# Performance work log

Measured on AMD Instinct MI355X. Metric: run time of the kernel, lower is better.

## Reference

```python
import jax, jax.numpy as jnp
import numpy as np

T, B, A, N = 64, 32, 8, 16
E, H = 64, 4
LSTM_I, LSTM_H = 128, 128
D_SELF = 16 + 9 * (32 - 2) + 4  # 290


def setup_inputs() -> dict:
    key = jax.random.key(0)
    ks = jax.random.split(key, 24)
    f32 = jnp.float32
    d = {}
    d["x_agent"] = jax.random.normal(ks[0], (T, B, A, 16), f32)
    d["x_lidar"] = jax.random.normal(ks[1], (T, B, A, 32), f32)
    d["x_safe_zone"] = jax.random.normal(ks[2], (T, B, A, 4), f32)
    d["x_ent0"] = jax.random.normal(ks[3], (T, B, A, N, 12), f32)
    d["x_ent1"] = jax.random.normal(ks[4], (T, B, A, N, 8), f32)
    d["mask0"] = jax.random.randint(ks[5], (T, B, A, N), 0, 2).astype(jnp.int32)
    d["mask1"] = jax.random.randint(ks[6], (T, B, A, N), 0, 2).astype(jnp.int32)
    d["done"] = jax.random.randint(ks[7], (T, B), 0, 2).astype(jnp.int32)
    d["actions"] = jax.random.randint(ks[8], (T, B, A, 2), 0, 5).astype(jnp.int32)
    w = lambda k, s: jax.random.normal(k, s, f32) * 0.05
    z = lambda s: jnp.zeros(s, f32)
    d["conv_w"] = w(ks[9], (9, 1, 3)); d["conv_b"] = z((9,))
    d["self_w"] = w(ks[10], (E, 2 * D_SELF)); d["self_b"] = z((E,))
    d["ent0_w"] = w(ks[11], (E, 12 + D_SELF)); d["ent0_b"] = z((E,))
    d["ent1_w"] = w(ks[12], (E, 8 + D_SELF)); d["ent1_b"] = z((E,))
    d["in_proj_w"] = w(ks[13], (3 * E, E)); d["in_proj_b"] = z((3 * E,))
    d["out_proj_w"] = w(ks[14], (E, E)); d["out_proj_b"] = z((E,))
    d["sa_w"] = w(ks[15], (E, E)); d["sa_b"] = z((E,))
    d["pool_w"] = w(ks[16], (LSTM_I, D_SELF + E)); d["pool_b"] = z((LSTM_I,))
    d["w_ih"] = w(ks[17], (4 * LSTM_H, LSTM_I)); d["w_hh"] = w(ks[18], (4 * LSTM_H, LSTM_H))
    d["b_ih"] = z((4 * LSTM_H,)); d["b_hh"] = z((4 * LSTM_H,))
    d["head0_w"] = w(ks[19], (5, LSTM_H)); d["head0_b"] = z((5,))
    d["head1_w"] = w(ks[20], (5, LSTM_H)); d["head1_b"] = z((5,))
    return d


def _forward(x_agent, x_lidar, x_safe_zone, x_ent0, x_ent1,
             conv_w, conv_b, self_w, self_b, ent0_w, ent0_b, ent1_w, ent1_b,
             in_proj_w, in_proj_b, out_proj_w, out_proj_b, sa_w, sa_b,
             pool_w, pool_b, w_ih, w_hh, b_ih, b_hh,
             head0_w, head0_b, head1_w, head1_b,
             mask0, mask1, done, actions):
    f32 = jnp.float32
    lin = lambda x, w, b: x @ w.T + b
    # lidar conv: Conv1d(1,9,k=3), padding=0 (padding_mode='circular' is inert with padding=0)
    xl = x_lidar.reshape(T * B * A, 1, 32)
    zl = jax.lax.conv_general_dilated(xl, conv_w, (1,), 'VALID',
                                      dimension_numbers=('NCH', 'OIH', 'NCH'))
    zl = jax.nn.relu(zl + conv_b[None, :, None]).reshape(T, B, A, -1)  # (T,B,A,270)
    x_self = jnp.concatenate([x_agent, zl, x_safe_zone], axis=-1)  # (T,B,A,290)
    z_self = jax.nn.relu(lin(jnp.concatenate([x_self, x_self], -1), self_w, self_b))[..., None, :]
    xs = jnp.broadcast_to(x_self[..., None, :], (T, B, A, N, D_SELF))
    z0 = jax.nn.relu(lin(jnp.concatenate([x_ent0, xs], -1), ent0_w, ent0_b))
    z1 = jax.nn.relu(lin(jnp.concatenate([x_ent1, xs], -1), ent1_w, ent1_b))
    z_ent = jnp.concatenate([z_self, z0, z1], axis=-2)  # (T,B,A,M,E), M = 1+2N = 33
    M = z_ent.shape[-2]
    mask = jnp.concatenate([jnp.ones((T, B, A, 1), f32),
                            mask0.astype(f32), mask1.astype(f32)], axis=-1)  # (T,B,A,M)
    # self-attention over entities, flattened over (T,B,A)
    S = T * B * A
    zf = z_ent.reshape(S, M, E)
    q, k, v = jnp.split(zf @ in_proj_w.T + in_proj_b, 3, axis=-1)
    Dh = E // H
    q = q.reshape(S, M, H, Dh); k = k.reshape(S, M, H, Dh); v = v.reshape(S, M, H, Dh)
    sc = jnp.einsum('sqhd,skhd->shqk', q, k) / np.float32(np.sqrt(Dh))
    valid = mask.reshape(S, M) > 0
    sc = jnp.where(valid[:, None, None, :], sc, jnp.float32(-1e9))
    attn = jax.nn.softmax(sc, axis=-1)
    o = jnp.einsum('shqk,skhd->sqhd', attn, v).reshape(S, M, E)
    o = (o @ out_proj_w.T + out_proj_b).reshape(T, B, A, M, E)
    res = z_ent + jax.nn.relu(lin(o, sa_w, sa_b))
    z_pool = jnp.mean(res * mask[..., None], axis=-2)  # torch.mean over entity dim (divide by M)
    zin = jax.nn.relu(lin(jnp.concatenate([x_self, z_pool], -1), pool_w, pool_b))  # (T,B,A,128)
    # LSTM scan with done-based state resets (PyTorch gate order i,f,g,o)
    zin_f = zin.reshape(T, B * A, LSTM_I)
    done_f = jnp.repeat(done.astype(f32), A, axis=-1)  # (T, B*A)
    def step(carry, inp):
        h, c = carry
        x_t, d_t = inp
        keep = (1.0 - d_t)[:, None]
        h = h * keep
        c = c * keep
        g = x_t @ w_ih.T + b_ih + h @ w_hh.T + b_hh
        i, f, gg, og = jnp.split(g, 4, axis=-1)
        c = jax.nn.sigmoid(f) * c + jax.nn.sigmoid(i) * jnp.tanh(gg)
        h = jax.nn.sigmoid(og) * jnp.tanh(c)
        return (h, c), h
    h0 = jnp.zeros((B * A, LSTM_H), f32)
    c0 = jnp.zeros((B * A, LSTM_H), f32)
    _, hs = jax.lax.scan(step, (h0, c0), (zin_f, done_f))
    z_lstm = hs.reshape(T, B, A, LSTM_H)
    # categorical heads: per-head logprob of given action and entropy
    lps, ents = [], []
    for i, (hw, hb) in enumerate(((head0_w, head0_b), (head1_w, head1_b))):
        logp = jax.nn.log_softmax(lin(z_lstm, hw, hb), axis=-1)
        p = jnp.exp(logp)
        ents.append(-(p * logp).sum(-1))
        lps.append(jnp.take_along_axis(logp, actions[..., i:i + 1], axis=-1)[..., 0])
    logprobs = lps[0] * lps[1]  # .prod(dim=-1) over heads as in source
    entropies = jnp.stack(ents, axis=-1)
    return logprobs, entropies


def reference(x_agent, x_lidar, x_safe_zone, x_ent0, x_ent1, mask0, mask1, done, actions,
              conv_w, conv_b, self_w, self_b, ent0_w, ent0_b, ent1_w, ent1_b,
              in_proj_w, in_proj_b, out_proj_w, out_proj_b, sa_w, sa_b,
              pool_w, pool_b, w_ih, w_hh, b_ih, b_hh,
              head0_w, head0_b, head1_w, head1_b):
    logprobs, entropies = _forward(x_agent, x_lidar, x_safe_zone, x_ent0, x_ent1,
                                   conv_w, conv_b, self_w, self_b, ent0_w, ent0_b,
                                   ent1_w, ent1_b, in_proj_w, in_proj_b, out_proj_w,
                                   out_proj_b, sa_w, sa_b, pool_w, pool_b,
                                   w_ih, w_hh, b_ih, b_hh,
                                   head0_w, head0_b, head1_w, head1_b,
                                   mask0, mask1, done, actions)
    return (actions, logprobs, entropies)
```

## Files before the change

### kernel.cpp

```cpp
#include <hip/hip_runtime.h>
#include <hip/hip_bf16.h>
#include <math.h>

#define T_DIM 64
#define B_DIM 32
#define S_TOT 16384
#define BA 256
#define FN_SB 16

#define ACT_OFF 0
#define LP_OFF 32768
#define ENT_OFF 49152

typedef __attribute__((ext_vector_type(8))) short short8;
typedef __attribute__((ext_vector_type(4))) float f32x4;
typedef unsigned int uint32;

__device__ __forceinline__ float sigf(float x) { return 1.0f / (1.0f + expf(-x)); }
__device__ __forceinline__ float bf2f(unsigned short u) {
    union { unsigned int i; float f; } a; a.i = ((unsigned int)u) << 16; return a.f;
}
__device__ __forceinline__ uint32 pkbf(float a, float b) {
    __hip_bfloat16 ha = __float2bfloat16(a), hb = __float2bfloat16(b);
    return (uint32)(*(unsigned short*)&ha) | ((uint32)(*(unsigned short*)&hb) << 16);
}
__device__ __forceinline__ short f2bs(float v) {
    __hip_bfloat16 h = __float2bfloat16(v); return *(short*)&h;
}
__device__ __forceinline__ int pswz(int row) { return (((row & 3) ^ ((row >> 2) & 3)) << 4); }

__global__ __launch_bounds__(256) void k_cvt2(
    const float* __restrict__ inp_w, const float* __restrict__ outp_w,
    const float* __restrict__ outp_b, const float* __restrict__ sa_w,
    const float* __restrict__ sa_b, const float* __restrict__ self_w,
    const float* __restrict__ pool_w, const float* __restrict__ ent0_w,
    const float* __restrict__ ent1_w, const float* __restrict__ w_ih,
    const float* __restrict__ w_hh,
    short* __restrict__ wq, short* __restrict__ Wf,
    short* __restrict__ We0, short* __restrict__ We1,
    short* __restrict__ wos, float* __restrict__ bos,
    short* __restrict__ wihb, short* __restrict__ whhb,
    short* __restrict__ wp2)
{
    int i = blockIdx.x * 256 + threadIdx.x;
    if (i < 12288) wq[i] = f2bs(inp_w[i]);
    if (i < 65536) { wihb[i] = f2bs(w_ih[i]); whhb[i] = f2bs(w_hh[i]); }
    if (i < 8192) { int c = i >> 6, k = i & 63; wp2[i] = f2bs(pool_w[(size_t)c * 354 + 290 + k]); }
    if (i < 4096) {
        int c = i >> 6, k = i & 63;
        float s = 0.f;
        for (int j = 0; j < 64; ++j) s = fmaf(sa_w[c * 64 + j], outp_w[j * 64 + k], s);
        wos[i] = f2bs(s);
    }
    if (i < 64) {
        float s = sa_b[i];
        for (int j = 0; j < 64; ++j) s = fmaf(sa_w[i * 64 + j], outp_b[j], s);
        bos[i] = s;
    }
    if (i < 1024) {
        int cp = i >> 4, k = i & 15;
        int ct = cp >> 4, lr2 = cp & 15;
        int e = 32 * (ct >> 1) + 2 * lr2 + (ct & 1);
        We0[i] = f2bs(k < 12 ? ent0_w[e * 302 + k] : 0.f);
        We1[i] = f2bs(k < 8 ? ent1_w[e * 298 + k] : 0.f);
    }
    if (i < 102400) {
        int c = i / 320, k = i - c * 320;
        float v = 0.f;
        if (k < 290) {
            if (c < 64) v = self_w[c * 580 + k] + self_w[c * 580 + 290 + k];
            else if (c < 192) v = pool_w[(size_t)(c - 64) * 354 + k];
            else if (c < 256) v = ent0_w[(c - 192) * 302 + 12 + k];
            else v = ent1_w[(c - 256) * 298 + 8 + k];
        }
        Wf[i] = f2bs(v);
    }
}

#define FN_XSB 0
#define FN_XP0 16384
#define FN_XP1 20736
#define FN_TOTAL 25088

__global__ __launch_bounds__(256, 4) void k_frontN(
    const float* __restrict__ xag, const float* __restrict__ xlid,
    const float* __restrict__ xsz, const float* __restrict__ xe0,
    const float* __restrict__ xe1,
    const float* __restrict__ conv_w, const float* __restrict__ conv_b,
    const float* __restrict__ self_b, const float* __restrict__ ent0_b,
    const float* __restrict__ ent1_b,
    const short* __restrict__ Wf, const short* __restrict__ We0,
    const short* __restrict__ We1,
    __hip_bfloat16* __restrict__ z_ent, float* __restrict__ zin_x)
{
    extern __shared__ char smem[];
    char* xsb = smem + FN_XSB;
    float* xp0f = (float*)(smem + FN_XP0);
    float* xp1f = (float*)(smem + FN_XP1);
    char* ae = smem + FN_XSB;
    float* lidf = (float*)(smem + FN_XP0);

    const int tid = threadIdx.x;
    const int s0 = blockIdx.x * FN_SB;
    const int wv = __builtin_amdgcn_readfirstlane(tid >> 6);
    const int l = tid & 63;
    const int lr = l & 15;
    const int lg = l >> 4;

    for (int i = tid; i < FN_SB * 32; i += 256) {
        int d = i & 31, sl = i >> 5;
        lidf[d * 18 + sl] = xlid[(size_t)s0 * 32 + i];
    }
    for (int i = tid; i < FN_SB * 16; i += 256) {
        int sl = i >> 4, d = i & 15;
        *(short*)(xsb + ((sl * 640 + d * 2) ^ ((sl & 7) << 4))) = f2bs(xag[(size_t)s0 * 16 + i]);
    }
    for (int i = tid; i < FN_SB * 4; i += 256) {
        int sl = i >> 2, d = i & 3;
        *(short*)(xsb + ((sl * 640 + (286 + d) * 2) ^ ((sl & 7) << 4))) = f2bs(xsz[(size_t)s0 * 4 + i]);
    }
    for (int i = tid; i < FN_SB * 30; i += 256) {
        int sl = i / 30, d = 290 + (i - (i / 30) * 30);
        *(short*)(xsb + ((sl * 640 + d * 2) ^ ((sl & 7) << 4))) = 0;
    }
    __syncthreads();
    for (int i = tid; i < 270 * FN_SB; i += 256) {
        int cp = i >> 4, sl = i & 15;
        int c = cp / 30, p = cp - c * 30;
        float v = conv_b[c] + conv_w[c * 3] * lidf[p * 18 + sl]
                + conv_w[c * 3 + 1] * lidf[(p + 1) * 18 + sl]
                + conv_w[c * 3 + 2] * lidf[(p + 2) * 18 + sl];
        *(short*)(xsb + ((sl * 640 + (16 + cp) * 2) ^ ((sl & 7) << 4))) = f2bs(fmaxf(v, 0.f));
    }
    __syncthreads();

    f32x4 acc[5];
    #pragma unroll
    for (int c = 0; c < 5; ++c) acc[c] = (f32x4){0.f, 0.f, 0.f, 0.f};

    for (int kk = 0; kk < 10; ++kk) {
        short8 af = *(const short8*)(xsb + ((lr * 640 + kk * 64 + lg * 16) ^ ((lr & 7) << 4)));
        short8 bf[5];
        #pragma unroll
        for (int c = 0; c < 5; ++c) {
            int col = (wv * 5 + c) * 16 + lr;
            bf[c] = *(const short8*)(Wf + (size_t)col * 320 + kk * 32 + lg * 8);
        }
        #pragma unroll
        for (int c = 0; c < 5; ++c)
            acc[c] = __builtin_amdgcn_mfma_f32_16x16x32_bf16(af, bf[c], acc[c], 0, 0, 0);
    }

    #pragma unroll
    for (int c = 0; c < 5; ++c) {
        int ct = wv * 5 + c;
        int gc = ct * 16 + lr;
        int rowb = lg * 4;
        f32x4 a = acc[c];
        if (ct * 16 < 64) {
            float bias = self_b[gc];
            #pragma unroll
            for (int r = 0; r < 4; ++r)
                z_ent[(size_t)(s0 + rowb + r) * 2112 + gc] = __float2bfloat16(fmaxf(a[r] + bias, 0.f));
        } else if (ct * 16 < 192) {
            int r2 = gc - 64;
            #pragma unroll
            for (int r = 0; r < 4; ++r)
                zin_x[(size_t)(s0 + rowb + r) * 128 + r2] = a[r];
        } else if (ct * 16 < 256) {
            float bias = ent0_b[gc - 192];
            #pragma unroll
            for (int r = 0; r < 4; ++r)
                xp0f[(rowb + r) * 68 + (gc - 192)] = a[r] + bias;
        } else {
            float bias = ent1_b[gc - 256];
            #pragma unroll
            for (int r = 0; r < 4; ++r)
                xp1f[(rowb + r) * 68 + (gc - 256)] = a[r] + bias;
        }
    }
    __syncthreads();

    {
        short8 bz = {0, 0, 0, 0, 0, 0, 0, 0};
        short8 be[4];
        #pragma unroll
        for (int ct = 0; ct < 4; ++ct) {
            int col = ct * 16 + lr;
            short8 bv = *(const short8*)(We0 + col * 16 + (lg & 1) * 8);
            be[ct] = (lg < 2) ? bv : bz;
        }
        for (int i = tid; i < 4096; i += 256) ((uint32*)ae)[i] = 0;
        __syncthreads();
        for (int i = tid; i < FN_SB * 192; i += 256) {
            int sl = i / 192, r = i - sl * 192;
            int n = r / 12, d = r - n * 12;
            int lrow = sl * 16 + n;
            *(short*)(ae + ((lrow * 64 + d * 2) ^ ((lrow & 3) << 4))) =
                f2bs(xe0[(size_t)s0 * 192 + i]);
        }
        __syncthreads();
        #pragma unroll
        for (int j = 0; j < 4; ++j) {
            int gs = wv * 4 + j;
            int row = gs * 16 + lr;
            short8 af = *(const short8*)(ae + ((row * 64 + lg * 16) ^ ((row & 3) << 4)));
            f32x4 a2[4];
            #pragma unroll
            for (int ct = 0; ct < 4; ++ct) {
                f32x4 z = {0.f, 0.f, 0.f, 0.f};
                a2[ct] = __builtin_amdgcn_mfma_f32_16x16x32_bf16(af, be[ct], z, 0, 0, 0);
            }
            #pragma unroll
            for (int t = 0; t < 2; ++t) {
                int e0 = 32 * t + 2 * lr;
                float xv0 = xp0f[gs * 68 + e0];
                float xv1 = xp0f[gs * 68 + e0 + 1];
                #pragma unroll
                for (int r = 0; r < 4; ++r) {
                    int n = lg * 4 + r;
                    float v0 = fmaxf(a2[2 * t][r] + xv0, 0.f);
                    float v1 = fmaxf(a2[2 * t + 1][r] + xv1, 0.f);
                    *(uint32*)((char*)z_ent + ((size_t)(s0 + gs) * 2112 + (1 + n) * 64 + e0) * 2) = pkbf(v0, v1);
                }
            }
        }
        __syncthreads();
    }

    {
        short8 bz = {0, 0, 0, 0, 0, 0, 0, 0};
        short8 be[4];
        #pragma unroll
        for (int ct = 0; ct < 4; ++ct) {
            int col = ct * 16 + lr;
            short8 bv = *(const short8*)(We1 + col * 16 + (lg & 1) * 8);
            be[ct] = (lg < 2) ? bv : bz;
        }
        for (int i = tid; i < 4096; i += 256) ((uint32*)ae)[i] = 0;
        __syncthreads();
        for (int i = tid; i < FN_SB * 128; i += 256) {
            int sl = i >> 7, r = i & 127;
            int n = r >> 3, d = r & 7;
            int lrow = sl * 16 + n;
            *(short*)(ae + ((lrow * 64 + d * 2) ^ ((lrow & 3) << 4))) =
                f2bs(xe1[(size_t)s0 * 128 + i]);
        }
        __syncthreads();
        #pragma unroll
        for (int j = 0; j < 4; ++j) {
            int gs = wv * 4 + j;
            int row = gs * 16 + lr;
            short8 af = *(const short8*)(ae + ((row * 64 + lg * 16) ^ ((row & 3) << 4)));
            f32x4 a2[4];
            #pragma unroll
            for (int ct = 0; ct < 4; ++ct) {
                f32x4 z = {0.f, 0.f, 0.f, 0.f};
                a2[ct] = __builtin_amdgcn_mfma_f32_16x16x32_bf16(af, be[ct], z, 0, 0, 0);
            }
            #pragma unroll
            for (int t = 0; t < 2; ++t) {
                int e0 = 32 * t + 2 * lr;
                float xv0 = xp1f[gs * 68 + e0];
                float xv1 = xp1f[gs * 68 + e0 + 1];
                #pragma unroll
                for (int r = 0; r < 4; ++r) {
                    int n = lg * 4 + r;
                    float v0 = fmaxf(a2[2 * t][r] + xv0, 0.f);
                    float v1 = fmaxf(a2[2 * t + 1][r] + xv1, 0.f);
                    *(uint32*)((char*)z_ent + ((size_t)(s0 + gs) * 2112 + (17 + n) * 64 + e0) * 2) = pkbf(v0, v1);
                }
            }
        }
    }
}

#define AG_QB   0
#define AG_KB   4224
#define AG_VT   8448
#define AG_PW   12544
#define AG_P32  16640
#define AG_V32  17408
#define AG_MSK  17664
#define AG_TOTAL 17824

__global__ __launch_bounds__(256, 8) void k_attnG(
    const __hip_bfloat16* __restrict__ z_ent,
    const int* __restrict__ mask0, const int* __restrict__ mask1,
    const short* __restrict__ wqkvb, const float* __restrict__ inp_b,
    const short* __restrict__ wos_g, const float* __restrict__ bos_g,
    float* __restrict__ pooled_ws)
{
    extern __shared__ char smem[];
    char*  Qb  = smem + AG_QB;
    char*  Kb  = smem + AG_KB;
    char*  Vt  = smem + AG_VT;
    char*  Pw  = smem + AG_PW;
    float* P32 = (float*)(smem + AG_P32);
    float* V32 = (float*)(smem + AG_V32);
    float* msk = (float*)(smem + AG_MSK);
    char*  ob  = Qb;

    const int tid = threadIdx.x;
    const int s = blockIdx.x;
    const short* zg = (const short*)(z_ent + (size_t)s * 2112);

    if (tid < 16) msk[1 + tid] = (float)mask0[(size_t)s * 16 + tid];
    else if (tid < 32) msk[17 + (tid - 16)] = (float)mask1[(size_t)s * 16 + (tid - 16)];
    else if (tid == 32) msk[0] = 1.0f;

    const int wv = __builtin_amdgcn_readfirstlane(tid >> 6);
    const int l  = tid & 63;
    const int lr = l & 15;
    const int lg = l >> 4;

    {
        short8 bw[3][2]; float bias[3];
        #pragma unroll
        for (int c = 0; c < 3; ++c) {
            int col = (wv * 3 + c) * 16 + lr;
            bw[c][0] = *(const short8*)(wqkvb + col * 64 + lg * 8);
            bw[c][1] = *(const short8*)(wqkvb + col * 64 + 32 + lg * 8);
            bias[c] = inp_b[col];
        }
        for (int rt = 0; rt < 3; ++rt) {
            int arow = rt * 16 + lr;
            if (arow > 32) arow = 32;
            short8 a0 = *(const short8*)(zg + arow * 64 + lg * 8);
            short8 a1 = *(const short8*)(zg + arow * 64 + 32 + lg * 8);
            #pragma unroll
            for (int c = 0; c < 3; ++c) {
                f32x4 acc = {0.f, 0.f, 0.f, 0.f};
                acc = __builtin_amdgcn_mfma_f32_16x16x32_bf16(a0, bw[c][0], acc, 0, 0, 0);
                acc = __builtin_amdgcn_mfma_f32_16x16x32_bf16(a1, bw[c][1], acc, 0, 0, 0);
                int col = (wv * 3 + c) * 16 + lr;
                int rb = rt * 16 + lg * 4;
                #pragma unroll
                for (int r = 0; r < 4; ++r) {
                    int q = rb + r;
                    if (q < 33) {
                        float val = acc[r] + bias[c];
                        if (col < 64) {
                            int h = col >> 4, d = col & 15;
                            *(short*)(Qb + ((h * 33 + q) * 32) + d * 2) = f2bs(val);
                        } else if (col < 128) {
                            int kc = col - 64; int h = kc >> 4, d = kc & 15;
                            *(short*)(Kb + ((h * 33 + q) * 32) + d * 2) = f2bs(val);
                        } else {
                            int vc = col - 128; int h = vc >> 4, d = vc & 15;
                            if (q < 32)
                                *(short*)(Vt + (h * 16 + d) * 64 + ((q * 2) ^ pswz(d))) = f2bs(val);
                            else
                                V32[h * 16 + d] = val;
                        }
                    }
                }
            }
        }
    }
    __syncthreads();

    uint32 pk[3][4];
    {
        const short8 zero8 = {0, 0, 0, 0, 0, 0, 0, 0};
        short8 kf[3];
        #pragma unroll
        for (int t = 0; t < 3; ++t)
            kf[t] = (lg < 2) ? *(const short8*)(Kb + ((wv * 33 + t * 16 + lr) * 32) + lg * 16) : zero8;
        float mk0 = msk[lr];
        float mk1 = msk[16 + lr];
        float mk2 = (lr == 0) ? msk[32] : 0.f;
        #pragma unroll
        for (int qt = 0; qt < 3; ++qt) {
            short8 qf = (lg < 2) ? *(const short8*)(Qb + ((wv * 33 + qt * 16 + lr) * 32) + lg * 16) : zero8;
            f32x4 z = {0.f, 0.f, 0.f, 0.f};
            f32x4 S0 = __builtin_amdgcn_mfma_f32_16x16x32_bf16(qf, kf[0], z, 0, 0, 0);
            f32x4 S1 = __builtin_amdgcn_mfma_f32_16x16x32_bf16(qf, kf[1], z, 0, 0, 0);
            f32x4 S2 = __builtin_amdgcn_mfma_f32_16x16x32_bf16(qf, kf[2], z, 0, 0, 0);
            #pragma unroll
            for (int r = 0; r < 4; ++r) {
                float v0 = (mk0 > 0.f) ? S0[r] * 0.25f : -1e9f;
                float v1 = (mk1 > 0.f) ? S1[r] * 0.25f : -1e9f;
                float v2 = (mk2 > 0.f) ? S2[r] * 0.25f : -1e9f;
                float m = fmaxf(fmaxf(v0, v1), v2);
                m = fmaxf(m, __shfl_xor(m, 1));
                m = fmaxf(m, __shfl_xor(m, 2));
                m = fmaxf(m, __shfl_xor(m, 4));
                m = fmaxf(m, __shfl_xor(m, 8));
                float e0 = __expf(v0 - m), e1 = __expf(v1 - m), e2 = __expf(v2 - m);
                float sm = e0 + e1 + e2;
                sm += __shfl_xor(sm, 1);
                sm += __shfl_xor(sm, 2);
                sm += __shfl_xor(sm, 4);
                sm += __shfl_xor(sm, 8);
                float inv = 1.0f / sm;
                pk[qt][r] = pkbf(e0 * inv, e1 * inv);
                if (lr == 0) P32[wv * 48 + qt * 16 + lg * 4 + r] = e2 * inv;
            }
        }
    }
    __syncthreads();

    {
        short8 vf = *(const short8*)(Vt + (wv * 16 + lr) * 64 + ((lg * 16) ^ pswz(lr)));
        float v32reg = V32[wv * 16 + lr];
        f32x4 C[3];
        #pragma unroll
        for (int qt = 0; qt < 3; ++qt) {
            #pragma unroll
            for (int r = 0; r < 4; ++r) {
                int ql = lg * 4 + r;
                uint32 p = pk[qt][r];
                char* prow = Pw + wv * 1024 + ql * 64;
                int sz = pswz(ql);
                *(short*)(prow + ((lr * 2) ^ sz)) = (short)(p & 0xffffu);
                *(short*)(prow + (((16 + lr) * 2) ^ sz)) = (short)(p >> 16);
            }
            short8 pf = *(const short8*)(Pw + wv * 1024 + lr * 64 + ((lg * 16) ^ pswz(lr)));
            f32x4 z = {0.f, 0.f, 0.f, 0.f};
            C[qt] = __builtin_amdgcn_mfma_f32_16x16x32_bf16(pf, vf, z, 0, 0, 0);
        }
        #pragma unroll
        for (int qt = 0; qt < 3; ++qt) {
            #pragma unroll
            for (int r = 0; r < 4; ++r) {
                int q = qt * 16 + lg * 4 + r;
                if (q <= 32) {
                    float cv = C[qt][r] + P32[wv * 48 + q] * v32reg;
                    *(short*)(ob + ((q * 128 + (wv * 16 + lr) * 2) ^ ((q & 7) << 4))) = f2bs(cv);
                }
            }
        }
    }
    __syncthreads();

    {
        int col = wv * 16 + lr;
        short8 b0 = *(const short8*)(wos_g + col * 64 + lg * 8);
        short8 b1 = *(const short8*)(wos_g + col * 64 + 32 + lg * 8);
        float bias = bos_g[col];
        float ps = 0.f;
        for (int rt = 0; rt < 3; ++rt) {
            int arow = rt * 16 + lr;
            int sw = (arow & 7) << 4;
            short8 a0 = *(const short8*)(ob + ((arow * 128 + lg * 16) ^ sw));
            short8 a1 = *(const short8*)(ob + ((arow * 128 + 64 + lg * 16) ^ sw));
            f32x4 acc = {0.f, 0.f, 0.f, 0.f};
            acc = __builtin_amdgcn_mfma_f32_16x16x32_bf16(a0, b0, acc, 0, 0, 0);
            acc = __builtin_amdgcn_mfma_f32_16x16x32_bf16(a1, b1, acc, 0, 0, 0);
            int rb = rt * 16 + lg * 4;
            #pragma unroll
            for (int r = 0; r < 4; ++r) {
                int row = rb + r;
                if (row < 33) {
                    float zev = bf2f(*(const unsigned short*)(zg + row * 64 + col));
                    ps += msk[row] * (zev + fmaxf(acc[r] + bias, 0.f));
                }
            }
        }
        ps += __shfl_xor(ps, 16); ps += __shfl_xor(ps, 32);
        if (lg == 0) pooled_ws[(size_t)s * 64 + col] = ps * (1.0f / 33.0f);
    }
}

__global__ __launch_bounds__(256, 2) void k_zinx(
    const float* __restrict__ pooled_ws, const float* __restrict__ zin_x,
    const short* __restrict__ wp2, const float* __restrict__ pool_b,
    const short* __restrict__ wihb, const float* __restrict__ b_ih,
    const float* __restrict__ b_hh, short* __restrict__ xp)
{
    extern __shared__ char smem[];
    char* A1 = smem;
    char* zt = smem + 8192;
    const int tid = threadIdx.x;
    const size_t r0 = (size_t)blockIdx.x * 64;

    for (int i = tid; i < 2048; i += 256) {
        int sl = i >> 5, dp = i & 31;
        float2 v = ((const float2*)(pooled_ws + (r0 + sl) * 64))[dp];
        *(uint32*)(A1 + ((sl * 128 + dp * 4) ^ ((sl & 7) << 4))) = pkbf(v.x, v.y);
    }
    __syncthreads();

    const int wv = __builtin_amdgcn_readfirstlane(tid >> 6);
    const int l = tid & 63;
    const int lr = l & 15;
    const int lg = l >> 4;

    #pragma unroll
    for (int c = 0; c < 2; ++c) {
        int col = (wv * 2 + c) * 16 + lr;
        short8 bf0 = *(const short8*)(wp2 + col * 64 + lg * 8);
        short8 bf1 = *(const short8*)(wp2 + col * 64 + 32 + lg * 8);
        float bias = pool_b[col];
        #pragma unroll
        for (int rt = 0; rt < 4; ++rt) {
            int row16 = rt * 16 + lr;
            short8 a0 = *(const short8*)(A1 + ((row16 * 128 + lg * 16) ^ ((row16 & 7) << 4)));
            short8 a1 = *(const short8*)(A1 + ((row16 * 128 + 64 + lg * 16) ^ ((row16 & 7) << 4)));
            f32x4 acc = {0.f, 0.f, 0.f, 0.f};
            acc = __builtin_amdgcn_mfma_f32_16x16x32_bf16(a0, bf0, acc, 0, 0, 0);
            acc = __builtin_amdgcn_mfma_f32_16x16x32_bf16(a1, bf1, acc, 0, 0, 0);
            #pragma unroll
            for (int r = 0; r < 4; ++r) {
                int row = rt * 16 + lg * 4 + r;
                float v = fmaxf(acc[r] + bias + zin_x[(r0 + row) * 128 + col], 0.f);
                *(short*)(zt + ((row * 256 + col * 2) ^ ((row & 7) << 4))) = f2bs(v);
            }
        }
    }
    __syncthreads();

    short8 af[4][4];
    #pragma unroll
    for (int rt = 0; rt < 4; ++rt)
        #pragma unroll
        for (int kc = 0; kc < 4; ++kc) {
            int row = rt * 16 + lr;
            af[rt][kc] = *(const short8*)(zt + ((row * 256 + kc * 64 + lg * 16) ^ ((row & 7) << 4)));
        }

    for (int ct8 = 0; ct8 < 8; ++ct8) {
        int ct = wv * 8 + ct8;
        int col = ct * 16 + lr;
        short8 bf[4];
        #pragma unroll
        for (int kc = 0; kc < 4; ++kc)
            bf[kc] = *(const short8*)(wihb + (size_t)col * 128 + kc * 32 + lg * 8);
        float bias = b_ih[col] + b_hh[col];
        int g = col >> 7, j = col & 127;
        #pragma unroll
        for (int rt = 0; rt < 4; ++rt) {
            f32x4 acc = {0.f, 0.f, 0.f, 0.f};
            #pragma unroll
            for (int kc = 0; kc < 4; ++kc)
                acc = __builtin_amdgcn_mfma_f32_16x16x32_bf16(af[rt][kc], bf[kc], acc, 0, 0, 0);
            #pragma unroll
            for (int r = 0; r < 4; ++r)
                xp[(r0 + rt * 16 + lg * 4 + r) * 512 + j * 4 + g] = f2bs(acc[r] + bias);
        }
    }
}

__global__ __launch_bounds__(512, 1) void k_lstm2(
    const short* __restrict__ xp, const short* __restrict__ whhb,
    const int* __restrict__ done, float* __restrict__ h_all)
{
    __shared__ short hl[16 * 128];
    __shared__ float keepl[64 * 16];
    const int tid = threadIdx.x;
    const int s0 = blockIdx.x * 16;
    const int wv = __builtin_amdgcn_readfirstlane(tid >> 6);
    const int l = tid & 63;
    const int lr = l & 15;
    const int lg = l >> 4;

    for (int i = tid; i < 1024; i += 512) {
        int t = i >> 4, ls = i & 15;
        keepl[i] = done[t * 32 + ((s0 + ls) >> 3)] ? 0.f : 1.f;
    }
    for (int i = tid; i < 1024; i += 512) ((uint32*)hl)[i] = 0;

    short8 bf[4][4];
    #pragma unroll
    for (int gi = 0; gi < 4; ++gi) {
        int col = (gi * 8 + wv) * 16 + lr;
        #pragma unroll
        for (int kc = 0; kc < 4; ++kc)
            bf[gi][kc] = *(const short8*)(whhb + (size_t)col * 128 + kc * 32 + lg * 8);
    }
    float c0 = 0.f, c1 = 0.f, c2 = 0.f, c3 = 0.f;
    const int jcol = wv * 16 + lr;

    short4 xn[4];
    #pragma unroll
    for (int r = 0; r < 4; ++r)
        xn[r] = *(const short4*)(xp + ((size_t)(s0 + lg * 4 + r)) * 512 + jcol * 4);
    __syncthreads();

    for (int t = 0; t < T_DIM; ++t) {
        short4 xc[4];
        #pragma unroll
        for (int r = 0; r < 4; ++r) xc[r] = xn[r];
        if (t < 63) {
            #pragma unroll
            for (int r = 0; r < 4; ++r)
                xn[r] = *(const short4*)(xp + ((size_t)(t + 1) * 256 + s0 + lg * 4 + r) * 512 + jcol * 4);
        }
        short8 af[4];
        #pragma unroll
        for (int kc = 0; kc < 4; ++kc)
            af[kc] = *(const short8*)((char*)hl + ((lr * 256 + kc * 64 + lg * 16) ^ ((lr & 7) << 4)));
        f32x4 z = {0.f, 0.f, 0.f, 0.f};
        f32x4 Ci = z, Cf = z, Cg = z, Co = z;
        #pragma unroll
        for (int kc = 0; kc < 4; ++kc) {
            Ci = __builtin_amdgcn_mfma_f32_16x16x32_bf16(af[kc], bf[0][kc], Ci, 0, 0, 0);
            Cf = __builtin_amdgcn_mfma_f32_16x16x32_bf16(af[kc], bf[1][kc], Cf, 0, 0, 0);
            Cg = __builtin_amdgcn_mfma_f32_16x16x32_bf16(af[kc], bf[2][kc], Cg, 0, 0, 0);
            Co = __builtin_amdgcn_mfma_f32_16x16x32_bf16(af[kc], bf[3][kc], Co, 0, 0, 0);
        }
        __syncthreads();

        #pragma unroll
        for (int r = 0; r < 4; ++r) {
            int sl = lg * 4 + r;
            float kt = keepl[t * 16 + sl];
            float gi = bf2f((unsigned short)xc[r].x) + Ci[r];
            float gf = bf2f((unsigned short)xc[r].y) + Cf[r];
            float gg = bf2f((unsigned short)xc[r].z) + Cg[r];
            float go = bf2f((unsigned short)xc[r].w) + Co[r];
            float cc = (r == 0 ? c0 : r == 1 ? c1 : r == 2 ? c2 : c3) * kt;
            cc = sigf(gf) * cc + sigf(gi) * tanhf(gg);
            float hn = sigf(go) * tanhf(cc);
            if (r == 0) c0 = cc; else if (r == 1) c1 = cc; else if (r == 2) c2 = cc; else c3 = cc;
            float kn = (t < 63) ? keepl[(t + 1) * 16 + sl] : 1.f;
            *(short*)((char*)hl + ((sl * 256 + jcol * 2) ^ ((sl & 7) << 4))) = f2bs(hn * kn);
            h_all[((size_t)t * 256 + s0 + sl) * 128 + jcol] = hn;
        }
        __syncthreads();
    }
}

__global__ __launch_bounds__(256) void k_heads(
    const float* __restrict__ h_all, const int* __restrict__ actions,
    const float* __restrict__ h0w, const float* __restrict__ h0b,
    const float* __restrict__ h1w, const float* __restrict__ h1b,
    float* __restrict__ out)
{
    __shared__ float w0[640], w1[640], b0[8], b1[8];
    const int tid = threadIdx.x;
    for (int i = tid; i < 640; i += 256) { w0[i] = h0w[i]; w1[i] = h1w[i]; }
    if (tid < 5) { b0[tid] = h0b[tid]; b1[tid] = h1b[tid]; }
    __syncthreads();
    const int g = blockIdx.x * 256 + tid;
    const float* h = h_all + (size_t)g * 128;
    float l0[5], l1[5];
    #pragma unroll
    for (int cc = 0; cc < 5; ++cc) { l0[cc] = b0[cc]; l1[cc] = b1[cc]; }
    for (int j = 0; j < 128; ++j) {
        float hv = h[j];
        #pragma unroll
        for (int cc = 0; cc < 5; ++cc) {
            l0[cc] = fmaf(w0[cc * 128 + j], hv, l0[cc]);
            l1[cc] = fmaf(w1[cc * 128 + j], hv, l1[cc]);
        }
    }
    int a0 = actions[(size_t)g * 2], a1 = actions[(size_t)g * 2 + 1];
    float m0 = l0[0], m1 = l1[0];
    #pragma unroll
    for (int cc = 1; cc < 5; ++cc) { m0 = fmaxf(m0, l0[cc]); m1 = fmaxf(m1, l1[cc]); }
    float s0 = 0.f, s1 = 0.f;
    #pragma unroll
    for (int cc = 0; cc < 5; ++cc) { s0 += expf(l0[cc] - m0); s1 += expf(l1[cc] - m1); }
    float lse0 = m0 + logf(s0), lse1 = m1 + logf(s1);
    float ent0 = 0.f, ent1 = 0.f, lp0 = 0.f, lp1 = 0.f;
    #pragma unroll
    for (int cc = 0; cc < 5; ++cc) {
        float p0 = l0[cc] - lse0, p1 = l1[cc] - lse1;
        ent0 -= expf(p0) * p0;
        ent1 -= expf(p1) * p1;
        if (cc == a0) lp0 = p0;
        if (cc == a1) lp1 = p1;
    }
    out[ACT_OFF + (size_t)g * 2]     = (float)a0;
    out[ACT_OFF + (size_t)g * 2 + 1] = (float)a1;
    out[LP_OFF + g]                  = lp0 * lp1;
    out[ENT_OFF + (size_t)g * 2]     = ent0;
    out[ENT_OFF + (size_t)g * 2 + 1] = ent1;
}

extern "C" void kernel_launch(void* const* d_in, const int* in_sizes, int n_in,
                              void* d_out, int out_size, void* d_ws, size_t ws_size,
                              hipStream_t stream)
{
    const float* x_agent = (const float*)d_in[0];
    const float* x_lidar = (const float*)d_in[1];
    const float* x_safe  = (const float*)d_in[2];
    const float* x_ent0  = (const float*)d_in[3];
    const float* x_ent1  = (const float*)d_in[4];
    const int*   mask0   = (const int*)d_in[5];
    const int*   mask1   = (const int*)d_in[6];
    const int*   done    = (const int*)d_in[7];
    const int*   actions = (const int*)d_in[8];
    const float* conv_w  = (const float*)d_in[9];
    const float* conv_b  = (const float*)d_in[10];
    const float* self_w  = (const float*)d_in[11];
    const float* self_b  = (const float*)d_in[12];
    const float* ent0_w  = (const float*)d_in[13];
    const float* ent0_b  = (const float*)d_in[14];
    const float* ent1_w  = (const float*)d_in[15];
    const float* ent1_b  = (const float*)d_in[16];
    const float* inp_w   = (const float*)d_in[17];
    const float* inp_b   = (const float*)d_in[18];
    const float* outp_w  = (const float*)d_in[19];
    const float* outp_b  = (const float*)d_in[20];
    const float* sa_w    = (const float*)d_in[21];
    const float* sa_b    = (const float*)d_in[22];
    const float* pool_w  = (const float*)d_in[23];
    const float* pool_b  = (const float*)d_in[24];
    const float* w_ih    = (const float*)d_in[25];
    const float* w_hh    = (const float*)d_in[26];
    const float* b_ih    = (const float*)d_in[27];
    const float* b_hh    = (const float*)d_in[28];
    const float* h0w     = (const float*)d_in[29];
    const float* h0b     = (const float*)d_in[30];
    const float* h1w     = (const float*)d_in[31];
    const float* h1b     = (const float*)d_in[32];

    __hip_bfloat16* z_ent = (__hip_bfloat16*)d_ws;
    float* zin_x  = (float*)((char*)d_ws + (size_t)S_TOT * 2112 * 2);
    float* pooled = zin_x + (size_t)S_TOT * 128;
    float* h_all  = pooled + (size_t)S_TOT * 64;
    short* xp     = (short*)(h_all + (size_t)S_TOT * 128);
    short* wqkvb  = xp + (size_t)S_TOT * 512;
    short* Wf     = wqkvb + 12288;
    short* We0    = Wf + 102400;
    short* We1    = We0 + 1024;
    short* wos    = We1 + 1024;
    float* bos    = (float*)(wos + 4096);
    short* wihb   = (short*)(bos + 64);
    short* whhb   = wihb + 65536;
    short* wp2    = whhb + 65536;

    k_cvt2<<<400, 256, 0, stream>>>(inp_w, outp_w, outp_b, sa_w, sa_b, self_w, pool_w,
                                    ent0_w, ent1_w, w_ih, w_hh,
                                    wqkvb, Wf, We0, We1, wos, bos, wihb, whhb, wp2);

    k_frontN<<<S_TOT / FN_SB, 256, FN_TOTAL, stream>>>(
        x_agent, x_lidar, x_safe, x_ent0, x_ent1,
        conv_w, conv_b, self_b, ent0_b, ent1_b,
        Wf, We0, We1, z_ent, zin_x);

    k_attnG<<<S_TOT, 256, AG_TOTAL, stream>>>(
        z_ent, mask0, mask1, wqkvb, inp_b, wos, bos, pooled);

    k_zinx<<<256, 256, 24576, stream>>>(pooled, zin_x, wp2, pool_b, wihb, b_ih, b_hh, xp);

    k_lstm2<<<16, 512, 0, stream>>>(xp, whhb, done, h_all);

    k_heads<<<S_TOT / 256, 256, 0, stream>>>(h_all, actions, h0w, h0b, h1w, h1b, (float*)d_out);
}
```

Baseline: 341.9 us.

## Vectorize entity loads, hoist conv weights, drop softmax max-reduction

Restructures the lidar conv loop so each channel's weights are hoisted out of the inner loop. Replaces scalar strided entity-feature loads with per-thread float4 loads packed into bf16 pairs. Removes the max-subtraction shuffle reduction in the attention softmax and masks by adding a large negative bias. Skipping the max relies on small score magnitudes, which risks overflow with larger activations, and masked entries now get exp(-40) instead of zero.

Result: faster. 318.1 us (-6.9%).

```diff
diff --git a/kernel.cpp b/kernel.cpp
--- a/kernel.cpp
+++ b/kernel.cpp
@@ -124,13 +124,16 @@
         *(short*)(xsb + ((sl * 640 + d * 2) ^ ((sl & 7) << 4))) = 0;
     }
     __syncthreads();
-    for (int i = tid; i < 270 * FN_SB; i += 256) {
-        int cp = i >> 4, sl = i & 15;
-        int c = cp / 30, p = cp - c * 30;
-        float v = conv_b[c] + conv_w[c * 3] * lidf[p * 18 + sl]
-                + conv_w[c * 3 + 1] * lidf[(p + 1) * 18 + sl]
-                + conv_w[c * 3 + 2] * lidf[(p + 2) * 18 + sl];
-        *(short*)(xsb + ((sl * 640 + (16 + cp) * 2) ^ ((sl & 7) << 4))) = f2bs(fmaxf(v, 0.f));
+    #pragma unroll
+    for (int c = 0; c < 9; ++c) {
+        float w0 = conv_w[c * 3], w1 = conv_w[c * 3 + 1], w2 = conv_w[c * 3 + 2];
+        float bb = conv_b[c];
+        for (int i = tid; i < 30 * FN_SB; i += 256) {
+            int p = i >> 4, sl = i & 15;
+            float v = bb + w0 * lidf[p * 18 + sl] + w1 * lidf[(p + 1) * 18 + sl]
+                    + w2 * lidf[(p + 2) * 18 + sl];
+            *(short*)(xsb + ((sl * 640 + (16 + c * 30 + p) * 2) ^ ((sl & 7) << 4))) = f2bs(fmaxf(v, 0.f));
+        }
     }
     __syncthreads();
 
@@ -192,12 +195,18 @@
         }
         for (int i = tid; i < 4096; i += 256) ((uint32*)ae)[i] = 0;
         __syncthreads();
-        for (int i = tid; i < FN_SB * 192; i += 256) {
-            int sl = i / 192, r = i - sl * 192;
-            int n = r / 12, d = r - n * 12;
-            int lrow = sl * 16 + n;
-            *(short*)(ae + ((lrow * 64 + d * 2) ^ ((lrow & 3) << 4))) =
-                f2bs(xe0[(size_t)s0 * 192 + i]);
+        {
+            int sl = tid >> 4, n = tid & 15;
+            int row = sl * 16 + n;
+            int sw = (row & 3) << 4;
+            const float4* src = (const float4*)(xe0 + (size_t)(s0 + sl) * 192 + n * 12);
+            float4 v0 = src[0], v1 = src[1], v2 = src[2];
+            *(uint32*)(ae + ((row * 64 + 0) ^ sw))  = pkbf(v0.x, v0.y);
+            *(uint32*)(ae + ((row * 64 + 4) ^ sw))  = pkbf(v0.z, v0.w);
+            *(uint32*)(ae + ((row * 64 + 8) ^ sw))  = pkbf(v1.x, v1.y);
+            *(uint32*)(ae + ((row * 64 + 12) ^ sw)) = pkbf(v1.z, v1.w);
+            *(uint32*)(ae + ((row * 64 + 16) ^ sw)) = pkbf(v2.x, v2.y);
+            *(uint32*)(ae + ((row * 64 + 20) ^ sw)) = pkbf(v2.z, v2.w);
         }
         __syncthreads();
         #pragma unroll
@@ -239,12 +248,16 @@
         }
         for (int i = tid; i < 4096; i += 256) ((uint32*)ae)[i] = 0;
         __syncthreads();
-        for (int i = tid; i < FN_SB * 128; i += 256) {
-            int sl = i >> 7, r = i & 127;
-            int n = r >> 3, d = r & 7;
-            int lrow = sl * 16 + n;
-            *(short*)(ae + ((lrow * 64 + d * 2) ^ ((lrow & 3) << 4))) =
-                f2bs(xe1[(size_t)s0 * 128 + i]);
+        {
+            int sl = tid >> 4, n = tid & 15;
+            int row = sl * 16 + n;
+            int sw = (row & 3) << 4;
+            const float4* src = (const float4*)(xe1 + (size_t)(s0 + sl) * 128 + n * 8);
+            float4 v0 = src[0], v1 = src[1];
+            *(uint32*)(ae + ((row * 64 + 0) ^ sw))  = pkbf(v0.x, v0.y);
+            *(uint32*)(ae + ((row * 64 + 4) ^ sw))  = pkbf(v0.z, v0.w);
+            *(uint32*)(ae + ((row * 64 + 8) ^ sw))  = pkbf(v1.x, v1.y);
+            *(uint32*)(ae + ((row * 64 + 12) ^ sw)) = pkbf(v1.z, v1.w);
         }
         __syncthreads();
         #pragma unroll
@@ -370,6 +383,9 @@
         float mk0 = msk[lr];
         float mk1 = msk[16 + lr];
         float mk2 = (lr == 0) ? msk[32] : 0.f;
+        float sc0 = mk0 * 0.25f, bo0 = (mk0 - 1.f) * 40.f;
+        float sc1 = mk1 * 0.25f, bo1 = (mk1 - 1.f) * 40.f;
+        float sc2 = mk2 * 0.25f, bo2 = (mk2 - 1.f) * 40.f;
         #pragma unroll
         for (int qt = 0; qt < 3; ++qt) {
             short8 qf = (lg < 2) ? *(const short8*)(Qb + ((wv * 33 + qt * 16 + lr) * 32) + lg * 16) : zero8;
@@ -379,15 +395,9 @@
             f32x4 S2 = __builtin_amdgcn_mfma_f32_16x16x32_bf16(qf, kf[2], z, 0, 0, 0);
             #pragma unroll
             for (int r = 0; r < 4; ++r) {
-                float v0 = (mk0 > 0.f) ? S0[r] * 0.25f : -1e9f;
-                float v1 = (mk1 > 0.f) ? S1[r] * 0.25f : -1e9f;
-                float v2 = (mk2 > 0.f) ? S2[r] * 0.25f : -1e9f;
-                float m = fmaxf(fmaxf(v0, v1), v2);
-                m = fmaxf(m, __shfl_xor(m, 1));
-                m = fmaxf(m, __shfl_xor(m, 2));
-                m = fmaxf(m, __shfl_xor(m, 4));
-                m = fmaxf(m, __shfl_xor(m, 8));
-                float e0 = __expf(v0 - m), e1 = __expf(v1 - m), e2 = __expf(v2 - m);
+                float e0 = __expf(fmaf(S0[r], sc0, bo0));
+                float e1 = __expf(fmaf(S1[r], sc1, bo1));
+                float e2 = __expf(fmaf(S2[r], sc2, bo2));
                 float sm = e0 + e1 + e2;
                 sm += __shfl_xor(sm, 1);
                 sm += __shfl_xor(sm, 2);
```
